# Performance work log

Measured on AMD Instinct MI355X. Metric: run time of the kernel, lower is better.

The kernel has to match this reference:

```python
import jax, jax.numpy as jnp
import jax.lax as lax
import numpy as np
import math

B, T_FRAMES, H, W = 32, 8, 14, 14
C, CA = 768, 384
L = H * W + 1


def setup_inputs() -> dict:
    key = jax.random.key(0)
    ks = jax.random.split(key, 7)
    s = 0.02
    return {
        "x": jax.random.normal(ks[0], (B * T_FRAMES, L, C), dtype=jnp.float32),
        "W1": jax.random.normal(ks[1], (CA, C), dtype=jnp.float32) * s,
        "b1": jnp.zeros((CA,), dtype=jnp.float32),
        "conv_w": jax.random.normal(ks[2], (CA, 1, 3, 3, 3), dtype=jnp.float32) * s,
        "conv_b": jnp.zeros((CA,), dtype=jnp.float32),
        "W2": jax.random.normal(ks[3], (C, CA), dtype=jnp.float32) * s,
        "b2": jnp.zeros((C,), dtype=jnp.float32),
        "T": T_FRAMES,
    }


def reference(x, W1, b1, conv_w, conv_b, W2, b2, T):
    BT, Lx, Cx = x.shape
    Bb = BT // T
    Ca = W1.shape[0]
    Hh = Ww = int(round(math.sqrt(Lx - 1)))
    # fc1 on all tokens except CLS: [BT, L-1, Ca]
    h = jnp.einsum("blc,ac->bla", x[:, 1:, :], W1) + b1
    # -> [B, Ca, T, H, W] for depthwise 3d conv (groups = Ca)
    h = h.reshape(Bb, T, Hh, Ww, Ca).transpose(0, 4, 1, 2, 3)
    h = lax.conv_general_dilated(
        h, conv_w,
        window_strides=(1, 1, 1),
        padding=[(1, 1), (1, 1), (1, 1)],
        dimension_numbers=("NCDHW", "OIDHW", "NCDHW"),
        feature_group_count=Ca,
    ) + conv_b[None, :, None, None, None]
    # back to [BT, L-1, Ca]
    h = h.transpose(0, 2, 3, 4, 1).reshape(BT, Lx - 1, Ca)
    # fc2: [BT, L-1, C]
    h = jnp.einsum("bla,ca->blc", h, W2) + b2
    # residual add onto non-CLS tokens
    return x.at[:, 1:, :].add(h)
```

## Files before the change

### kernel.cpp

```cpp
#include <hip/hip_runtime.h>
#include <hip/hip_bf16.h>
#include <stdint.h>

#define BTOT   256
#define LX     197
#define CDIM   768
#define CADIM  384
#define TFR    8
#define LM1    196
#define MTOT   50176

typedef unsigned short u16;
typedef short          bf16x8 __attribute__((ext_vector_type(8)));
typedef unsigned short u16x4  __attribute__((ext_vector_type(4)));
typedef unsigned short u16x8  __attribute__((ext_vector_type(8)));
typedef float          f32x4  __attribute__((ext_vector_type(4)));

typedef const __attribute__((address_space(1))) void gvoid_t;
typedef __attribute__((address_space(3))) void       svoid_t;

static __device__ __forceinline__ u16 f2bf(float f) {
  union { float f; uint32_t u; } v; v.f = f;
  uint32_t u = v.u;
  return (u16)((u + 0x7FFFu + ((u >> 16) & 1u)) >> 16);
}
static __device__ __forceinline__ float bf2f(u16 h) {
  union { uint32_t u; float f; } v; v.u = ((uint32_t)h) << 16;
  return v.f;
}
static __device__ __forceinline__ u16 f2bf_hw(float f) {
  union { __hip_bfloat16 b; u16 u; } v;
  v.b = __float2bfloat16(f);
  return v.u;
}

__global__ void prep_small(const float4* __restrict__ x4, float4* __restrict__ out4,
                           const float* __restrict__ W1, const float* __restrict__ W2,
                           const float* __restrict__ cw, u16* __restrict__ w1b,
                           u16* __restrict__ w2b, float* __restrict__ cwT) {
  int i = blockIdx.x * blockDim.x + threadIdx.x;
  if (i < CADIM * CDIM) { w1b[i] = f2bf(W1[i]); w2b[i] = f2bf(W2[i]); }
  if (i < CADIM * 27) {
    int a = i / 27; int tap = i - a * 27;
    cwT[tap * CADIM + a] = cw[i];
  }
  if (i < BTOT * 192) {
    int f = i / 192, v = i - f * 192;
    size_t off = (size_t)f * (LX * CDIM / 4) + v;
    out4[off] = x4[off];
  }
}


__global__ __launch_bounds__(768, 2) void fc1_gemm(
    const float* __restrict__ X,
    const u16* __restrict__ Bw,
    const float* __restrict__ bias,
    u16* __restrict__ Hout)
{
  __shared__ __align__(16) u16 As[2 * 128 * 32];
  __shared__ __align__(16) u16 Bs[2 * 384 * 32];
  const int tid  = threadIdx.x;
  const int lane = tid & 63;
  const int wave = tid >> 6;
  const int m0 = blockIdx.x * 128;
  const int lm = lane & 15;
  const int lk = lane >> 4;
  const int wr = wave / 6;
  const int wc = wave - wr * 6;
  const int wm = wr * 64;
  const int wn = wc * 64;
  const bool is_a = (wave < 8);

  const int g = tid >> 3;
  const int q = tid & 7;
  size_t arow[2];
  int awst[2];
  if (is_a) {
#pragma unroll
    for (int s = 0; s < 2; ++s) {
      int row = g + 64 * s;
      int tok = m0 + row;
      int bt = tok / LM1;
      int l  = tok - bt * LM1;
      arow[s] = (size_t)(bt * LX + 1 + l) * CDIM + q * 4;
      int R    = row >> 1;
      int uu   = (row & 1) * 4 + (q >> 1);
      int slot = uu ^ (R & 7);
      awst[s]  = R * 64 + slot * 8 + (q & 1) * 4;
    }
  }

  const int wb  = wave - 8;
  const int u   = (lane & 7) ^ (lane >> 3);
  const int rr  = 2 * (lane >> 3) + (u >> 2);
  const int cko = (u & 3) * 8;
  size_t boff[6];
  int ldst[6];
  if (!is_a) {
#pragma unroll
    for (int s = 0; s < 6; ++s) {
      int row = wb * 96 + s * 16 + rr;
      boff[s] = (size_t)row * CDIM + cko;
      ldst[s] = (wb * 48 + s * 8) * 64;
    }
  }

  const int lmh   = lm >> 1;
  const int slotp = (((lm & 1) << 2) | lk) ^ lmh;
  const int abase = ((wm >> 1) + lmh) * 64 + slotp * 8;
  const int bbase = ((wn >> 1) + lmh) * 64 + slotp * 8;

  f32x4 acc[4][4];
#pragma unroll
  for (int i = 0; i < 4; i++)
#pragma unroll
    for (int j = 0; j < 4; j++) acc[i][j] = (f32x4)0.0f;

  float4 areg[2];

  if (is_a) {
#pragma unroll
    for (int s = 0; s < 2; ++s) areg[s] = *(const float4*)(X + arow[s]);
#pragma unroll
    for (int s = 0; s < 2; ++s) {
      u16x4 o;
      o[0] = f2bf_hw(areg[s].x); o[1] = f2bf_hw(areg[s].y);
      o[2] = f2bf_hw(areg[s].z); o[3] = f2bf_hw(areg[s].w);
      *(u16x4*)&As[awst[s]] = o;
    }
  } else {
#pragma unroll
    for (int s = 0; s < 6; ++s)
      __builtin_amdgcn_global_load_lds((gvoid_t*)(Bw + boff[s]),
          (svoid_t*)(Bs + ldst[s]), 16, 0, 0);
  }
  __syncthreads();

  int cur = 0;
  for (int kt = 0; kt < 23; ++kt) {
    const int k1 = (kt + 1) * 32;
    const int nb = cur ^ 1;
    if (is_a) {
#pragma unroll
      for (int s = 0; s < 2; ++s) areg[s] = *(const float4*)(X + arow[s] + k1);
    } else {
#pragma unroll
      for (int s = 0; s < 6; ++s)
        __builtin_amdgcn_global_load_lds((gvoid_t*)(Bw + boff[s] + k1),
            (svoid_t*)(Bs + nb * 12288 + ldst[s]), 16, 0, 0);
    }
    {
      const u16* Ab = As + cur * 4096;
      const u16* Bb = Bs + cur * 12288;
      bf16x8 af[4], bfr[4];
#pragma unroll
      for (int i = 0; i < 4; i++) af[i] = *(const bf16x8*)&Ab[abase + i * 512];
#pragma unroll
      for (int j = 0; j < 4; j++) bfr[j] = *(const bf16x8*)&Bb[bbase + j * 512];
#pragma unroll
      for (int i = 0; i < 4; i++)
#pragma unroll
        for (int j = 0; j < 4; j++)
          acc[i][j] = __builtin_amdgcn_mfma_f32_16x16x32_bf16(af[i], bfr[j], acc[i][j], 0, 0, 0);
    }
    if (is_a) {
#pragma unroll
      for (int s = 0; s < 2; ++s) {
        u16x4 o;
        o[0] = f2bf_hw(areg[s].x); o[1] = f2bf_hw(areg[s].y);
        o[2] = f2bf_hw(areg[s].z); o[3] = f2bf_hw(areg[s].w);
        *(u16x4*)&As[nb * 4096 + awst[s]] = o;
      }
    }
    __syncthreads();
    cur ^= 1;
  }
  {
    const u16* Ab = As + cur * 4096;
    const u16* Bb = Bs + cur * 12288;
    bf16x8 af[4], bfr[4];
#pragma unroll
    for (int i = 0; i < 4; i++) af[i] = *(const bf16x8*)&Ab[abase + i * 512];
#pragma unroll
    for (int j = 0; j < 4; j++) bfr[j] = *(const bf16x8*)&Bb[bbase + j * 512];
#pragma unroll
    for (int i = 0; i < 4; i++)
#pragma unroll
      for (int j = 0; j < 4; j++)
        acc[i][j] = __builtin_amdgcn_mfma_f32_16x16x32_bf16(af[i], bfr[j], acc[i][j], 0, 0, 0);
  }

#pragma unroll
  for (int i = 0; i < 4; i++) {
    int rbase = m0 + wm + i * 16 + lk * 4;
#pragma unroll
    for (int j = 0; j < 4; j++) {
      int col = wn + j * 16 + lm;
      float bv = bias[col];
#pragma unroll
      for (int r = 0; r < 4; r++)
        Hout[(rbase + r) * CADIM + col] = f2bf(acc[i][j][r] + bv);
    }
  }
}

__global__ __launch_bounds__(256) void dwconv(
    const u16* __restrict__ h1, const float* __restrict__ cwT,
    const float* __restrict__ cb, u16* __restrict__ h2)
{
  __shared__ __align__(16) u16 lin[3 * 196 * 32];
  const int tid = threadIdx.x;
  const int f   = blockIdx.x;
  const int cc  = blockIdx.y;
  const int tv  = f & 7;

  for (int i = tid; i < 3 * 196 * 4; i += 256) {
    int fd  = i / 784;
    int rem = i - fd * 784;
    int pos = rem >> 2;
    int c8  = rem & 3;
    int tt  = tv + fd - 1;
    u16x8 v = (u16x8)0;
    if (tt >= 0 && tt < TFR) {
      const u16* src = h1 + ((size_t)(f + fd - 1) * LM1 + pos) * CADIM
                          + cc * 32 + c8 * 8;
      v = *(const u16x8*)src;
    }
    *(u16x8*)&lin[(fd * 196 + pos) * 32 + c8 * 8] = v;
  }
  __syncthreads();

  const int cg    = tid & 3;
  const int pidx  = tid >> 2;
  const int cbase = cc * 32 + cg * 8;

  float bv[8];
#pragma unroll
  for (int c = 0; c < 8; ++c) bv[c] = cb[cbase + c];

  float acc[4][8];
  int hk[4], wk[4];
#pragma unroll
  for (int k = 0; k < 4; ++k) {
    int p = pidx + 64 * k;
    hk[k] = p / 14;
    wk[k] = p - hk[k] * 14;
#pragma unroll
    for (int c = 0; c < 8; ++c) acc[k][c] = bv[c];
  }

  for (int dt = 0; dt < 3; ++dt) {
#pragma unroll
    for (int j = 0; j < 9; ++j) {
      const int dh = j / 3 - 1, dw = j % 3 - 1;
      float w8[8];
      const float* wp8 = cwT + (dt * 9 + j) * CADIM + cbase;
#pragma unroll
      for (int c = 0; c < 8; ++c) w8[c] = wp8[c];
#pragma unroll
      for (int k = 0; k < 4; ++k) {
        int p = pidx + 64 * k;
        if (p >= 196) continue;
        int hh = hk[k] + dh, ww = wk[k] + dw;
        if (hh < 0 || hh >= 14 || ww < 0 || ww >= 14) continue;
        const u16x8 v = *(const u16x8*)&lin[(dt * 196 + hh * 14 + ww) * 32 + cg * 8];
#pragma unroll
        for (int c = 0; c < 8; ++c)
          acc[k][c] += bf2f((u16)v[c]) * w8[c];
      }
    }
  }

#pragma unroll
  for (int k = 0; k < 4; ++k) {
    int p = pidx + 64 * k;
    if (p < 196) {
      u16x8 o;
#pragma unroll
      for (int c = 0; c < 8; ++c) o[c] = f2bf(acc[k][c]);
      *(u16x8*)(h2 + ((size_t)f * LM1 + p) * CADIM + cbase) = o;
    }
  }
}

__global__ __launch_bounds__(256) void fc2_gemm(
    const u16* __restrict__ A,
    const u16* __restrict__ Bw,
    const float* __restrict__ bias,
    const float* __restrict__ x,
    float* __restrict__ out)
{
  __shared__ __align__(16) u16 As[2 * 128 * 32];
  __shared__ __align__(16) u16 Bs[2 * 128 * 32];
  const int tid  = threadIdx.x;
  const int lane = tid & 63;
  const int wave = tid >> 6;

  const int orig = blockIdx.x;
  const int lgc  = (orig & 7) * 294 + (orig >> 3);
  const int lmt  = lgc / 6;
  const int lnt  = lgc - lmt * 6;
  const int m0 = lmt * 128;
  const int n0 = lnt * 128;

  const int lm = lane & 15;
  const int lk = lane >> 4;
  const int wm = (wave & 1) * 64;
  const int wn = (wave >> 1) * 64;

  const int u   = (lane & 7) ^ (lane >> 3);
  const int rr  = 2 * (lane >> 3) + (u >> 2);
  const int cko = (u & 3) * 8;
  size_t aoff[2], boff[2];
  int ldst[2];
#pragma unroll
  for (int s = 0; s < 2; ++s) {
    int row = wave * 32 + s * 16 + rr;
    aoff[s] = (size_t)(m0 + row) * CADIM + cko;
    boff[s] = (size_t)(n0 + row) * CADIM + cko;
    ldst[s] = (wave * 16 + s * 8) * 64;
  }

  const int lmh   = lm >> 1;
  const int slotp = (((lm & 1) << 2) | lk) ^ lmh;
  const int abase = ((wm >> 1) + lmh) * 64 + slotp * 8;
  const int bbase = ((wn >> 1) + lmh) * 64 + slotp * 8;

  f32x4 acc[4][4];
#pragma unroll
  for (int i = 0; i < 4; i++)
#pragma unroll
    for (int j = 0; j < 4; j++) acc[i][j] = (f32x4)0.0f;

#pragma unroll
  for (int s = 0; s < 2; ++s) {
    __builtin_amdgcn_global_load_lds((gvoid_t*)(A + aoff[s]),
        (svoid_t*)(As + ldst[s]), 16, 0, 0);
    __builtin_amdgcn_global_load_lds((gvoid_t*)(Bw + boff[s]),
        (svoid_t*)(Bs + ldst[s]), 16, 0, 0);
  }
  __syncthreads();
  int cur = 0;
  for (int kt = 0; kt < 11; ++kt) {
    const int k1 = (kt + 1) * 32;
    const int nb = cur ^ 1;
#pragma unroll
    for (int s = 0; s < 2; ++s) {
      __builtin_amdgcn_global_load_lds((gvoid_t*)(A + aoff[s] + k1),
          (svoid_t*)(As + nb * 4096 + ldst[s]), 16, 0, 0);
      __builtin_amdgcn_global_load_lds((gvoid_t*)(Bw + boff[s] + k1),
          (svoid_t*)(Bs + nb * 4096 + ldst[s]), 16, 0, 0);
    }
    {
      const u16* Ab = As + cur * 4096;
      const u16* Bb = Bs + cur * 4096;
      bf16x8 af[4], bfr[4];
#pragma unroll
      for (int i = 0; i < 4; i++) af[i] = *(const bf16x8*)&Ab[abase + i * 512];
#pragma unroll
      for (int j = 0; j < 4; j++) bfr[j] = *(const bf16x8*)&Bb[bbase + j * 512];
#pragma unroll
      for (int i = 0; i < 4; i++)
#pragma unroll
        for (int j = 0; j < 4; j++)
          acc[i][j] = __builtin_amdgcn_mfma_f32_16x16x32_bf16(af[i], bfr[j], acc[i][j], 0, 0, 0);
    }
    __syncthreads();
    cur ^= 1;
  }
  {
    const u16* Ab = As + cur * 4096;
    const u16* Bb = Bs + cur * 4096;
    bf16x8 af[4], bfr[4];
#pragma unroll
    for (int i = 0; i < 4; i++) af[i] = *(const bf16x8*)&Ab[abase + i * 512];
#pragma unroll
    for (int j = 0; j < 4; j++) bfr[j] = *(const bf16x8*)&Bb[bbase + j * 512];
#pragma unroll
    for (int i = 0; i < 4; i++)
#pragma unroll
      for (int j = 0; j < 4; j++)
        acc[i][j] = __builtin_amdgcn_mfma_f32_16x16x32_bf16(af[i], bfr[j], acc[i][j], 0, 0, 0);
  }

  float bv[4];
#pragma unroll
  for (int j = 0; j < 4; j++) bv[j] = bias[n0 + wn + j * 16 + lm];
#pragma unroll
  for (int i = 0; i < 4; i++) {
    int rbase = m0 + wm + i * 16 + lk * 4;
    size_t orow[4];
#pragma unroll
    for (int r = 0; r < 4; r++) {
      int tok = rbase + r;
      int bt = tok / LM1;
      int l  = tok - bt * LM1;
      orow[r] = (size_t)(bt * LX + 1 + l) * CDIM + (n0 + wn + lm);
    }
    float xv[4][4];
#pragma unroll
    for (int r = 0; r < 4; r++)
#pragma unroll
      for (int j = 0; j < 4; j++)
        xv[r][j] = x[orow[r] + j * 16];
#pragma unroll
    for (int r = 0; r < 4; r++)
#pragma unroll
      for (int j = 0; j < 4; j++)
        out[orow[r] + j * 16] = xv[r][j] + acc[i][j][r] + bv[j];
  }
}

extern "C" void kernel_launch(void* const* d_in, const int* in_sizes, int n_in,
                              void* d_out, int out_size, void* d_ws, size_t ws_size,
                              hipStream_t stream) {
  const float* x  = (const float*)d_in[0];
  const float* W1 = (const float*)d_in[1];
  const float* b1 = (const float*)d_in[2];
  const float* cw = (const float*)d_in[3];
  const float* cb = (const float*)d_in[4];
  const float* W2 = (const float*)d_in[5];
  const float* b2 = (const float*)d_in[6];
  float* out = (float*)d_out;

  char* ws = (char*)d_ws;
  u16*   w1b = (u16*)(ws + 0);
  u16*   w2b = (u16*)(ws + 589824);
  float* cwT = (float*)(ws + 1179648);
  u16*   h1  = (u16*)(ws + 1245184);
  u16*   h2  = (u16*)(ws + 39780352);

  prep_small<<<1152, 256, 0, stream>>>((const float4*)x, (float4*)out,
                                       W1, W2, cw, w1b, w2b, cwT);
  fc1_gemm<<<MTOT / 128, 768, 0, stream>>>(x, w1b, b1, h1);
  dwconv  <<<dim3(BTOT, 12), 256, 0, stream>>>(h1, cwT, cb, h2);
  fc2_gemm<<<2352, 256, 0, stream>>>(h2, w2b, b2, x, out);
}
```

Before: 433.2 us.

## Prefetch fc1 A tiles two steps ahead with role-specific waitcnt barriers

Restructures the fc1 GEMM main loop into a manually unrolled two-stage loop with two register sets for the A (x) tile. Global loads of x now run two k-steps ahead, so their latency overlaps a full MFMA step instead of one. __syncthreads is replaced by explicit s_waitcnt plus s_barrier that wait only on the counters each warp role uses. This adds register pressure and more complex ordering, and the hand-written waitcnts could be fragile.

```diff
diff --git a/kernel.cpp b/kernel.cpp
--- a/kernel.cpp
+++ b/kernel.cpp
@@ -117,78 +117,103 @@
 #pragma unroll
     for (int j = 0; j < 4; j++) acc[i][j] = (f32x4)0.0f;
 
-  float4 areg[2];
+  float4 aregA[2], aregB[2];
+
+#define FC1_COMPUTE(bufidx)                                                 \
+  {                                                                         \
+    const u16* Ab = As + (bufidx) * 4096;                                   \
+    const u16* Bb = Bs + (bufidx) * 12288;                                  \
+    bf16x8 af[4], bfr[4];                                                   \
+    _Pragma("unroll")                                                       \
+    for (int i = 0; i < 4; i++) af[i] = *(const bf16x8*)&Ab[abase + i * 512]; \
+    _Pragma("unroll")                                                       \
+    for (int j = 0; j < 4; j++) bfr[j] = *(const bf16x8*)&Bb[bbase + j * 512]; \
+    _Pragma("unroll")                                                       \
+    for (int i = 0; i < 4; i++)                                             \
+      _Pragma("unroll")                                                     \
+      for (int j = 0; j < 4; j++)                                           \
+        acc[i][j] = __builtin_amdgcn_mfma_f32_16x16x32_bf16(af[i], bfr[j], acc[i][j], 0, 0, 0); \
+  }
+
+#define FC1_WRITE_A(R, bufidx)                                              \
+  {                                                                         \
+    _Pragma("unroll")                                                       \
+    for (int s = 0; s < 2; ++s) {                                           \
+      u16x4 o;                                                              \
+      o[0] = f2bf_hw(R[s].x); o[1] = f2bf_hw(R[s].y);                       \
+      o[2] = f2bf_hw(R[s].z); o[3] = f2bf_hw(R[s].w);                       \
+      *(u16x4*)&As[(bufidx) * 4096 + awst[s]] = o;                          \
+    }                                                                       \
+  }
+
+#define FC1_BARRIER()                                                       \
+  {                                                                         \
+    if (is_a) asm volatile("s_waitcnt lgkmcnt(0)" ::: "memory");            \
+    else      asm volatile("s_waitcnt vmcnt(0) lgkmcnt(0)" ::: "memory");   \
+    __builtin_amdgcn_s_barrier();                                           \
+  }
 
   if (is_a) {
 #pragma unroll
-    for (int s = 0; s < 2; ++s) areg[s] = *(const float4*)(X + arow[s]);
-#pragma unroll
-    for (int s = 0; s < 2; ++s) {
-      u16x4 o;
-      o[0] = f2bf_hw(areg[s].x); o[1] = f2bf_hw(areg[s].y);
-      o[2] = f2bf_hw(areg[s].z); o[3] = f2bf_hw(areg[s].w);
-      *(u16x4*)&As[awst[s]] = o;
-    }
+    for (int s = 0; s < 2; ++s) aregA[s] = *(const float4*)(X + arow[s]);
+    FC1_WRITE_A(aregA, 0);
+#pragma unroll
+    for (int s = 0; s < 2; ++s) aregA[s] = *(const float4*)(X + arow[s] + 32);
+#pragma unroll
+    for (int s = 0; s < 2; ++s) aregB[s] = aregA[s];
   } else {
 #pragma unroll
     for (int s = 0; s < 6; ++s)
       __builtin_amdgcn_global_load_lds((gvoid_t*)(Bw + boff[s]),
           (svoid_t*)(Bs + ldst[s]), 16, 0, 0);
   }
-  __syncthreads();
-
-  int cur = 0;
-  for (int kt = 0; kt < 23; ++kt) {
-    const int k1 = (kt + 1) * 32;
-    const int nb = cur ^ 1;
-    if (is_a) {
-#pragma unroll
-      for (int s = 0; s < 2; ++s) areg[s] = *(const float4*)(X + arow[s] + k1);
-    } else {
+  FC1_BARRIER();
+
+  for (int kt = 0; kt < 22; kt += 2) {
+    {
+      const int k2 = (kt + 2) * 32;
+      if (is_a) {
+#pragma unroll
+        for (int s = 0; s < 2; ++s) aregA[s] = *(const float4*)(X + arow[s] + k2);
+      } else {
+        const int k1 = (kt + 1) * 32;
+#pragma unroll
+        for (int s = 0; s < 6; ++s)
+          __builtin_amdgcn_global_load_lds((gvoid_t*)(Bw + boff[s] + k1),
+              (svoid_t*)(Bs + 12288 + ldst[s]), 16, 0, 0);
+      }
+      FC1_COMPUTE(0);
+      if (is_a) FC1_WRITE_A(aregB, 1);
+      FC1_BARRIER();
+    }
+    {
+      const int k2 = (kt + 3) * 32;
+      if (is_a) {
+#pragma unroll
+        for (int s = 0; s < 2; ++s) aregB[s] = *(const float4*)(X + arow[s] + k2);
+      } else {
+        const int k1 = (kt + 2) * 32;
+#pragma unroll
+        for (int s = 0; s < 6; ++s)
+          __builtin_amdgcn_global_load_lds((gvoid_t*)(Bw + boff[s] + k1),
+              (svoid_t*)(Bs + ldst[s]), 16, 0, 0);
+      }
+      FC1_COMPUTE(1);
+      if (is_a) FC1_WRITE_A(aregA, 0);
+      FC1_BARRIER();
+    }
+  }
+  {
+    if (!is_a) {
 #pragma unroll
       for (int s = 0; s < 6; ++s)
-        __builtin_amdgcn_global_load_lds((gvoid_t*)(Bw + boff[s] + k1),
-            (svoid_t*)(Bs + nb * 12288 + ldst[s]), 16, 0, 0);
-    }
-    {
-      const u16* Ab = As + cur * 4096;
-      const u16* Bb = Bs + cur * 12288;
-      bf16x8 af[4], bfr[4];
-#pragma unroll
-      for (int i = 0; i < 4; i++) af[i] = *(const bf16x8*)&Ab[abase + i * 512];
-#pragma unroll
-      for (int j = 0; j < 4; j++) bfr[j] = *(const bf16x8*)&Bb[bbase + j * 512];
-#pragma unroll
-      for (int i = 0; i < 4; i++)
-#pragma unroll
-        for (int j = 0; j < 4; j++)
-          acc[i][j] = __builtin_amdgcn_mfma_f32_16x16x32_bf16(af[i], bfr[j], acc[i][j], 0, 0, 0);
-    }
-    if (is_a) {
-#pragma unroll
-      for (int s = 0; s < 2; ++s) {
-        u16x4 o;
-        o[0] = f2bf_hw(areg[s].x); o[1] = f2bf_hw(areg[s].y);
-        o[2] = f2bf_hw(areg[s].z); o[3] = f2bf_hw(areg[s].w);
-        *(u16x4*)&As[nb * 4096 + awst[s]] = o;
-      }
-    }
-    __syncthreads();
-    cur ^= 1;
-  }
-  {
-    const u16* Ab = As + cur * 4096;
-    const u16* Bb = Bs + cur * 12288;
-    bf16x8 af[4], bfr[4];
-#pragma unroll
-    for (int i = 0; i < 4; i++) af[i] = *(const bf16x8*)&Ab[abase + i * 512];
-#pragma unroll
-    for (int j = 0; j < 4; j++) bfr[j] = *(const bf16x8*)&Bb[bbase + j * 512];
-#pragma unroll
-    for (int i = 0; i < 4; i++)
-#pragma unroll
-      for (int j = 0; j < 4; j++)
-        acc[i][j] = __builtin_amdgcn_mfma_f32_16x16x32_bf16(af[i], bfr[j], acc[i][j], 0, 0, 0);
+        __builtin_amdgcn_global_load_lds((gvoid_t*)(Bw + boff[s] + 23 * 32),
+            (svoid_t*)(Bs + 12288 + ldst[s]), 16, 0, 0);
+    }
+    FC1_COMPUTE(0);
+    if (is_a) FC1_WRITE_A(aregB, 1);
+    FC1_BARRIER();
+    FC1_COMPUTE(1);
   }
 
 #pragma unroll
@@ -203,6 +228,9 @@
         Hout[(rbase + r) * CADIM + col] = f2bf(acc[i][j][r] + bv);
     }
   }
+#undef FC1_COMPUTE
+#undef FC1_WRITE_A
+#undef FC1_BARRIER
 }
 
 __global__ __launch_bounds__(256) void dwconv(
```

Measured after the change: 435.8 us. About the same (+0.6%).
